# Performance work log

Hardware: AMD Instinct MI355X
Metric: run time of the kernel (lower is better)

The kernel has to match this reference:

```python
import jax, jax.numpy as jnp
import numpy as np


def setup_inputs() -> dict:
    key = jax.random.key(0)
    k1, k2, k3, k4, k5 = jax.random.split(key, 5)
    B, C, G, H, W = 2, 64, 4, 64, 64
    CG = C * G            # 256 complex input channels (flattened)
    DQK = max(C // 8, 1)  # 8  query/key channels after gabor pooling
    scale = 1.0 / np.sqrt(CG)
    x = jax.random.normal(k1, (2, B, C, G, H, W), dtype=jnp.float32)
    wq = jax.random.normal(k2, (2, DQK, CG), dtype=jnp.float32) * scale
    wk = jax.random.normal(k3, (2, DQK, CG), dtype=jnp.float32) * scale
    wv = jax.random.normal(k4, (2, CG, CG), dtype=jnp.float32) * scale
    gamma = jax.random.normal(k5, (1,), dtype=jnp.float32) * 0.1
    return {"x": x, "wq": wq, "wk": wk, "wv": wv, "gamma": gamma}


def _cconv1x1(w, xr, xi):
    """Complex 1x1 conv: (wr+i wi)(xr+i xi). w: (2,O,Cin), x: (B,Cin,L)."""
    wr, wi = w[0], w[1]
    yr = jnp.einsum('oc,bcl->bol', wr, xr) - jnp.einsum('oc,bcl->bol', wi, xi)
    yi = jnp.einsum('oc,bcl->bol', wr, xi) + jnp.einsum('oc,bcl->bol', wi, xr)
    return yr, yi


def reference(x, wq, wk, wv, gamma):
    _, B, C, G, H, W = x.shape
    L = H * W
    xr = x[0].reshape(B, C * G, L)
    xi = x[1].reshape(B, C * G, L)
    # complex Q (B,d,L) / K (B,d,L)
    qr, qi = _cconv1x1(wq, xr, xi)
    kr, ki = _cconv1x1(wk, xr, xi)
    # energy = Q^H-free complex bmm: energy[b,l,m] = sum_d q[b,d,l] * k[b,d,m]
    er = jnp.einsum('bdl,bdm->blm', qr, kr) - jnp.einsum('bdl,bdm->blm', qi, ki)
    ei = jnp.einsum('bdl,bdm->blm', qr, ki) + jnp.einsum('bdl,bdm->blm', qi, kr)
    # magnitude-squared softmax over last axis -> real attention (B,L,L)
    att = jax.nn.softmax(er * er + ei * ei, axis=-1)
    # complex V (B,CG,L); out[b,c,m] = sum_l v[b,c,l] * att[b,m,l]
    vr, vi = _cconv1x1(wv, xr, xi)
    out_r = jnp.einsum('bcl,bml->bcm', vr, att)
    out_i = jnp.einsum('bcl,bml->bcm', vi, att)
    out = jnp.stack([out_r, out_i]).reshape(2, B, C, G, H, W)
    return gamma * out + x
```

## Files before the change

### kernel.cpp

```cpp
#include <hip/hip_runtime.h>
#include <cstdint>

constexpr int Bc  = 2;
constexpr int CGc = 256;
constexpr int Dc  = 8;
constexpr int Lc  = 4096;

typedef __attribute__((ext_vector_type(8))) short short8;
typedef __attribute__((ext_vector_type(4))) float floatx4;

__device__ inline unsigned short f2bf(float f) {
  union { float f; unsigned u; } v; v.f = f;
  unsigned r = v.u + 0x7fffu + ((v.u >> 16) & 1u);
  return (unsigned short)(r >> 16);
}
__device__ inline float bf2f(unsigned short h) {
  return __uint_as_float((unsigned)h << 16);
}

__global__ __launch_bounds__(256) void init_stats(float* __restrict__ p) {
  p[blockIdx.x * 256 + threadIdx.x] = 0.f;
}

__global__ __launch_bounds__(256) void wcat_pack(const float* __restrict__ wv,
                                                 unsigned short* __restrict__ Wcat) {
  const int i  = blockIdx.x * 256 + threadIdx.x;
  const int cc = i >> 9, k = i & 511;
  const int co = cc >> 8, c = cc & 255, ci = k >> 8, cin = k & 255;
  const float wr = wv[(size_t)c * CGc + cin];
  const float wi = wv[(size_t)(CGc + c) * CGc + cin];
  const float val = co == 0 ? (ci == 0 ? wr : -wi) : (ci == 0 ? wi : wr);
  Wcat[i] = f2bf(val);
}

__global__ __launch_bounds__(256) void xT_pack(const float* __restrict__ x,
                                               unsigned short* __restrict__ Xlk) {
  __shared__ float xs[64][65];
  const int tid = threadIdx.x;
  const int b   = blockIdx.z;
  const int l0  = blockIdx.x * 64;
  const int c0  = blockIdx.y * 64;
  const int lt  = tid & 63, r4 = tid >> 6;
#pragma unroll
  for (int p = 0; p < 16; ++p) {
    const int row  = p * 4 + r4;
    const int cin2 = c0 + row;
    const int comp = cin2 >> 8, cin = cin2 & 255;
    xs[row][lt] = x[((size_t)(comp * Bc + b) * CGc + cin) * Lc + l0 + lt];
  }
  __syncthreads();
#pragma unroll
  for (int p = 0; p < 16; ++p) {
    const int lr = p * 4 + r4;
    Xlk[((size_t)b * Lc + l0 + lr) * 512 + c0 + lt] = f2bf(xs[lt][lr]);
  }
}

__global__ __launch_bounds__(256) void qk_proj(const float* __restrict__ x,
                                               const float* __restrict__ wq,
                                               const float* __restrict__ wk,
                                               float* __restrict__ qout,
                                               float* __restrict__ kout) {
  __shared__ float ws[4 * Dc * CGc];
  const int tid = threadIdx.x;
  const int b   = blockIdx.y;
  for (int i = tid; i < 2 * Dc * CGc; i += 256) {
    ws[i]                 = wq[i];
    ws[2 * Dc * CGc + i]  = wk[i];
  }
  __syncthreads();
  const int d  = tid >> 5;
  const int ml = tid & 31;
  const int m  = blockIdx.x * 32 + ml;
  const float* xr = x + ((size_t)(0 * Bc + b) * CGc) * Lc + m;
  const float* xi = x + ((size_t)(1 * Bc + b) * CGc) * Lc + m;
  const float* wqr = ws + d * CGc;
  const float* wqi = ws + (Dc + d) * CGc;
  const float* wkr = ws + 2 * Dc * CGc + d * CGc;
  const float* wki = ws + 2 * Dc * CGc + (Dc + d) * CGc;
  float qer = 0.f, qei = 0.f, ker = 0.f, kei = 0.f;
#pragma unroll 4
  for (int cin = 0; cin < CGc; ++cin) {
    const float vr = xr[(size_t)cin * Lc];
    const float vi = xi[(size_t)cin * Lc];
    const float a1 = wqr[cin], b1 = wqi[cin];
    qer = fmaf(a1, vr, qer); qer = fmaf(-b1, vi, qer);
    qei = fmaf(a1, vi, qei); qei = fmaf(b1, vr, qei);
    const float a2 = wkr[cin], b2 = wki[cin];
    ker = fmaf(a2, vr, ker); ker = fmaf(-b2, vi, ker);
    kei = fmaf(a2, vi, kei); kei = fmaf(b2, vr, kei);
  }
  float* qp = qout + ((size_t)b * Lc + m) * 16;
  qp[d]     = qer;
  qp[8 + d] = qei;
  float* kp = kout + ((size_t)b * Lc + m) * 16;
  kp[d]     = ker;
  kp[8 + d] = kei;
}

__global__ __launch_bounds__(256) void qk_pack(const float* __restrict__ q,
                                               const float* __restrict__ k,
                                               unsigned short* __restrict__ Qcat,
                                               unsigned short* __restrict__ K1hi,
                                               unsigned short* __restrict__ K1lo,
                                               unsigned short* __restrict__ K2hi,
                                               unsigned short* __restrict__ K2lo) {
  const int r = blockIdx.x * 256 + threadIdx.x;
  {
    const float* qp = q + (size_t)r * 16;
    unsigned u[16];
#pragma unroll
    for (int t = 0; t < 8; ++t) {
      const float v0 = qp[2 * t], v1 = qp[2 * t + 1];
      const unsigned short h0 = f2bf(v0), h1 = f2bf(v1);
      u[t] = (unsigned)h0 | ((unsigned)h1 << 16);
      const unsigned short l0 = f2bf(v0 - bf2f(h0));
      const unsigned short l1 = f2bf(v1 - bf2f(h1));
      u[8 + t] = (unsigned)l0 | ((unsigned)l1 << 16);
    }
    uint4* dst = (uint4*)(Qcat + (size_t)r * 32);
    dst[0] = make_uint4(u[0], u[1], u[2], u[3]);
    dst[1] = make_uint4(u[4], u[5], u[6], u[7]);
    dst[2] = make_uint4(u[8], u[9], u[10], u[11]);
    dst[3] = make_uint4(u[12], u[13], u[14], u[15]);
  }
  {
    const float* kp = k + (size_t)r * 16;
    float k1[16], k2[16];
#pragma unroll
    for (int d = 0; d < 8; ++d) {
      const float kr = kp[d], ki = kp[8 + d];
      k1[d] = kr;  k1[8 + d] = -ki;
      k2[d] = ki;  k2[8 + d] = kr;
    }
    unsigned uh[8], ul[8];
#pragma unroll
    for (int t = 0; t < 8; ++t) {
      const unsigned short h0 = f2bf(k1[2 * t]), h1 = f2bf(k1[2 * t + 1]);
      uh[t] = (unsigned)h0 | ((unsigned)h1 << 16);
      const unsigned short l0 = f2bf(k1[2 * t] - bf2f(h0));
      const unsigned short l1 = f2bf(k1[2 * t + 1] - bf2f(h1));
      ul[t] = (unsigned)l0 | ((unsigned)l1 << 16);
    }
    uint4* dh = (uint4*)(K1hi + (size_t)r * 16);
    dh[0] = make_uint4(uh[0], uh[1], uh[2], uh[3]);
    dh[1] = make_uint4(uh[4], uh[5], uh[6], uh[7]);
    uint4* dl = (uint4*)(K1lo + (size_t)r * 16);
    dl[0] = make_uint4(ul[0], ul[1], ul[2], ul[3]);
    dl[1] = make_uint4(ul[4], ul[5], ul[6], ul[7]);
#pragma unroll
    for (int t = 0; t < 8; ++t) {
      const unsigned short h0 = f2bf(k2[2 * t]), h1 = f2bf(k2[2 * t + 1]);
      uh[t] = (unsigned)h0 | ((unsigned)h1 << 16);
      const unsigned short l0 = f2bf(k2[2 * t] - bf2f(h0));
      const unsigned short l1 = f2bf(k2[2 * t + 1] - bf2f(h1));
      ul[t] = (unsigned)l0 | ((unsigned)l1 << 16);
    }
    uint4* dh2 = (uint4*)(K2hi + (size_t)r * 16);
    dh2[0] = make_uint4(uh[0], uh[1], uh[2], uh[3]);
    dh2[1] = make_uint4(uh[4], uh[5], uh[6], uh[7]);
    uint4* dl2 = (uint4*)(K2lo + (size_t)r * 16);
    dl2[0] = make_uint4(ul[0], ul[1], ul[2], ul[3]);
    dl2[1] = make_uint4(ul[4], ul[5], ul[6], ul[7]);
  }
}

__global__ __launch_bounds__(256) void v_gemm(const unsigned short* __restrict__ Wcat,
                                              const unsigned short* __restrict__ Xlk,
                                              unsigned short* __restrict__ vbf) {
  __shared__ short As[128 * 64];
  __shared__ short Bs[64 * 64];
  const int tid  = threadIdx.x;
  const int b    = blockIdx.z;
  const int cc0  = blockIdx.x * 128;
  const int l0   = blockIdx.y * 64;
  const int wid  = tid >> 6, lane = tid & 63;
  const int wcc  = (wid >> 1) * 64;
  const int wl   = (wid & 1) * 32;
  const int lrow = lane & 15, quad = lane >> 4;
  floatx4 acc[4][2] = {};
  const unsigned short* wsrc = Wcat + (size_t)cc0 * 512;
  const unsigned short* xsrc = Xlk + ((size_t)b * Lc + l0) * 512;
  int s_off[4], g_off[4];
#pragma unroll
  for (int r = 0; r < 4; ++r) {
    const int idx = r * 256 + tid;
    const int row = idx >> 3, ch = idx & 7;
    s_off[r] = row * 64 + (ch ^ (row & 7)) * 8;
    g_off[r] = row * 512 + ch * 8;
  }
  short8 ar[4], br[2];
#pragma unroll
  for (int r = 0; r < 4; ++r) ar[r] = *(const short8*)(wsrc + g_off[r]);
#pragma unroll
  for (int r = 0; r < 2; ++r) br[r] = *(const short8*)(xsrc + g_off[r]);
  for (int k0 = 0; k0 < 512; k0 += 64) {
    __syncthreads();
#pragma unroll
    for (int r = 0; r < 4; ++r) *(short8*)&As[s_off[r]] = ar[r];
#pragma unroll
    for (int r = 0; r < 2; ++r) *(short8*)&Bs[s_off[r]] = br[r];
    __syncthreads();
    if (k0 + 64 < 512) {
#pragma unroll
      for (int r = 0; r < 4; ++r) ar[r] = *(const short8*)(wsrc + g_off[r] + k0 + 64);
#pragma unroll
      for (int r = 0; r < 2; ++r) br[r] = *(const short8*)(xsrc + g_off[r] + k0 + 64);
    }
#pragma unroll
    for (int kk = 0; kk < 64; kk += 32) {
      const int cb = kk >> 3;
      short8 af[4], bf[2];
#pragma unroll
      for (int i = 0; i < 4; ++i)
        af[i] = *(const short8*)&As[(wcc + i * 16 + lrow) * 64 +
                                    ((cb + quad) ^ (lrow & 7)) * 8];
#pragma unroll
      for (int j = 0; j < 2; ++j)
        bf[j] = *(const short8*)&Bs[(wl + j * 16 + lrow) * 64 +
                                    ((cb + quad) ^ (lrow & 7)) * 8];
#pragma unroll
      for (int i = 0; i < 4; ++i)
#pragma unroll
        for (int j = 0; j < 2; ++j)
          acc[i][j] = __builtin_amdgcn_mfma_f32_16x16x32_bf16(af[i], bf[j], acc[i][j], 0, 0, 0);
    }
  }
#pragma unroll
  for (int i = 0; i < 4; ++i) {
    const int ccb = cc0 + wcc + i * 16 + quad * 4;
#pragma unroll
    for (int j = 0; j < 2; ++j) {
      const int l = l0 + wl + j * 16 + lrow;
#pragma unroll
      for (int rg = 0; rg < 4; ++rg)
        vbf[((size_t)b * 512 + ccb + rg) * Lc + l] = f2bf(acc[i][j][rg]);
    }
  }
}

__global__ __launch_bounds__(256) void e_max(const unsigned short* __restrict__ Qcat,
                                             const unsigned short* __restrict__ K1hi,
                                             const unsigned short* __restrict__ K2hi,
                                             float* __restrict__ Mrow) {
  const int tid  = threadIdx.x;
  const int w    = tid >> 6, lane = tid & 63;
  const int lrow = lane & 15, quad = lane >> 4, qsel = quad & 1;
  const int b    = blockIdx.z;
  const int m16  = blockIdx.x * 64 + w * 16;
  const int lbeg = blockIdx.y * 512;
  const size_t kb = (size_t)b * Lc;
  const short8 afrag = *(const short8*)(Qcat + (kb + m16 + lrow) * 32 + quad * 8);
  float mx[4] = {0.f, 0.f, 0.f, 0.f};
  for (int l0 = lbeg; l0 < lbeg + 512; l0 += 16) {
    const size_t l = kb + l0 + lrow;
    const short8 b1h = *(const short8*)(K1hi + l * 16 + qsel * 8);
    const short8 b2h = *(const short8*)(K2hi + l * 16 + qsel * 8);
    const floatx4 er = __builtin_amdgcn_mfma_f32_16x16x32_bf16(afrag, b1h, (floatx4){0.f, 0.f, 0.f, 0.f}, 0, 0, 0);
    const floatx4 ei = __builtin_amdgcn_mfma_f32_16x16x32_bf16(afrag, b2h, (floatx4){0.f, 0.f, 0.f, 0.f}, 0, 0, 0);
#pragma unroll
    for (int r = 0; r < 4; ++r) {
      float e = er[r] * er[r];
      e = fmaf(ei[r], ei[r], e);
      mx[r] = fmaxf(mx[r], e);
    }
  }
#pragma unroll
  for (int r = 0; r < 4; ++r) {
    float v = mx[r];
#pragma unroll
    for (int off = 1; off < 16; off <<= 1) v = fmaxf(v, __shfl_xor(v, off));
    if (lrow == 0)
      atomicMax((unsigned*)&Mrow[kb + m16 + quad * 4 + r], __float_as_uint(v));
  }
}

__global__ __launch_bounds__(256) void e_exp(const unsigned short* __restrict__ Qcat,
                                             const unsigned short* __restrict__ K1hi,
                                             const unsigned short* __restrict__ K1lo,
                                             const unsigned short* __restrict__ K2hi,
                                             const unsigned short* __restrict__ K2lo,
                                             const float* __restrict__ Mrow,
                                             unsigned short* __restrict__ att,
                                             float* __restrict__ Ssum) {
  const int tid  = threadIdx.x;
  const int w    = tid >> 6, lane = tid & 63;
  const int lrow = lane & 15, quad = lane >> 4, qsel = quad & 1;
  const int b    = blockIdx.z;
  const int m16  = blockIdx.x * 64 + w * 16;
  const int lbeg = blockIdx.y * 512;
  const size_t kb = (size_t)b * Lc;
  const short8 afrag = *(const short8*)(Qcat + (kb + m16 + lrow) * 32 + quad * 8);
  float Mv[4], sum[4] = {};
#pragma unroll
  for (int r = 0; r < 4; ++r) Mv[r] = Mrow[kb + m16 + quad * 4 + r];
  for (int l0 = lbeg; l0 < lbeg + 512; l0 += 16) {
    const size_t l = kb + l0 + lrow;
    const short8 b1h = *(const short8*)(K1hi + l * 16 + qsel * 8);
    const short8 b1l = *(const short8*)(K1lo + l * 16 + qsel * 8);
    const short8 b2h = *(const short8*)(K2hi + l * 16 + qsel * 8);
    const short8 b2l = *(const short8*)(K2lo + l * 16 + qsel * 8);
    floatx4 er = __builtin_amdgcn_mfma_f32_16x16x32_bf16(afrag, b1l, (floatx4){0.f, 0.f, 0.f, 0.f}, 0, 0, 0);
    er = __builtin_amdgcn_mfma_f32_16x16x32_bf16(afrag, b1h, er, 0, 0, 0);
    floatx4 ei = __builtin_amdgcn_mfma_f32_16x16x32_bf16(afrag, b2l, (floatx4){0.f, 0.f, 0.f, 0.f}, 0, 0, 0);
    ei = __builtin_amdgcn_mfma_f32_16x16x32_bf16(afrag, b2h, ei, 0, 0, 0);
#pragma unroll
    for (int r = 0; r < 4; ++r) {
      float e = er[r] * er[r];
      e = fmaf(ei[r], ei[r], e);
      const float wgt = __expf(e - Mv[r]);
      sum[r] += wgt;
      att[(kb + m16 + quad * 4 + r) * Lc + l0 + lrow] = f2bf(wgt);
    }
  }
#pragma unroll
  for (int r = 0; r < 4; ++r) {
    float v = sum[r];
#pragma unroll
    for (int off = 1; off < 16; off <<= 1) v += __shfl_xor(v, off);
    if (lrow == 0) atomicAdd(&Ssum[kb + m16 + quad * 4 + r], v);
  }
}

__device__ __forceinline__ void pv_compute(const short* __restrict__ As,
                                           const short* __restrict__ Bs,
                                           int wcc, int wm, int lrow, int quad,
                                           floatx4 (&acc)[4][4]) {
#pragma unroll
  for (int kk = 0; kk < 64; kk += 32) {
    const int cb = kk >> 3;
    short8 af[4], bf[4];
#pragma unroll
    for (int i = 0; i < 4; ++i)
      af[i] = *(const short8*)&As[(wcc + i * 16 + lrow) * 64 +
                                  ((cb + quad) ^ (lrow & 7)) * 8];
#pragma unroll
    for (int j = 0; j < 4; ++j)
      bf[j] = *(const short8*)&Bs[(wm + j * 16 + lrow) * 64 +
                                  ((cb + quad) ^ (lrow & 7)) * 8];
#pragma unroll
    for (int i = 0; i < 4; ++i)
#pragma unroll
      for (int j = 0; j < 4; ++j)
        acc[i][j] = __builtin_amdgcn_mfma_f32_16x16x32_bf16(af[i], bf[j], acc[i][j], 0, 0, 0);
  }
}

__global__ __launch_bounds__(512, 2) void pv_gemm(const unsigned short* __restrict__ v,
                                                  const unsigned short* __restrict__ att,
                                                  const float* __restrict__ Ssum,
                                                  const float* __restrict__ x,
                                                  const float* __restrict__ gamma,
                                                  float* __restrict__ out) {
  __shared__ short smem[4 * 128 * 64];
  const int flat = blockIdx.x;
  const int swz  = (flat & 7) * 32 + (flat >> 3);
  const int b    = swz >> 7;
  const int rem  = swz & 127;
  const int m0   = (rem >> 2) * 128;
  const int cc0  = (rem & 3) * 128;
  const int tid  = threadIdx.x;
  const int wid  = tid >> 6, lane = tid & 63;
  const int g    = wid >> 2;
  const int w4   = wid & 3;
  const int wcc  = (w4 >> 1) * 64;
  const int wm   = (w4 & 1) * 64;
  const int lrow = lane & 15, quad = lane >> 4;
  floatx4 acc[4][4] = {};
  const unsigned short* vsrc = v   + ((size_t)b * 512 + cc0) * Lc;
  const unsigned short* asrc = att + ((size_t)b * Lc + m0) * Lc;
  int s_off[2];
  size_t g_off[2];
#pragma unroll
  for (int r = 0; r < 2; ++r) {
    const int c   = r * 512 + tid;
    const int row = c >> 3, ch = c & 7;
    s_off[r] = row * 64 + (ch ^ (row & 7)) * 8;
    g_off[r] = (size_t)row * Lc + ch * 8;
  }
  short8 ar[2][2], br[2][2];
#pragma unroll
  for (int p = 0; p < 2; ++p)
#pragma unroll
    for (int r = 0; r < 2; ++r) {
      ar[p][r] = *(const short8*)(vsrc + g_off[r] + p * 64);
      br[p][r] = *(const short8*)(asrc + g_off[r] + p * 64);
    }
  for (int k0 = 0; k0 < Lc; k0 += 128) {
    __syncthreads();
#pragma unroll
    for (int p = 0; p < 2; ++p)
#pragma unroll
      for (int r = 0; r < 2; ++r) {
        *(short8*)&smem[p * 8192 + s_off[r]]         = ar[p][r];
        *(short8*)&smem[16384 + p * 8192 + s_off[r]] = br[p][r];
      }
    __syncthreads();
    if (k0 + 128 < Lc) {
#pragma unroll
      for (int p = 0; p < 2; ++p)
#pragma unroll
        for (int r = 0; r < 2; ++r) {
          ar[p][r] = *(const short8*)(vsrc + g_off[r] + k0 + 128 + p * 64);
          br[p][r] = *(const short8*)(asrc + g_off[r] + k0 + 128 + p * 64);
        }
    }
    pv_compute(smem + g * 8192, smem + 16384 + g * 8192, wcc, wm, lrow, quad, acc);
  }
  __syncthreads();
  float* red = (float*)smem;
  if (g == 1) {
#pragma unroll
    for (int i = 0; i < 4; ++i)
#pragma unroll
      for (int j = 0; j < 4; ++j) {
        const int tq = i * 4 + j;
        *(floatx4*)&red[((w4 * 64 + lane) * 16 + (tq ^ (lane & 15))) * 4] = acc[i][j];
      }
  }
  __syncthreads();
  if (g == 0) {
#pragma unroll
    for (int i = 0; i < 4; ++i)
#pragma unroll
      for (int j = 0; j < 4; ++j) {
        const int tq = i * 4 + j;
        const floatx4 o = *(const floatx4*)&red[((w4 * 64 + lane) * 16 + (tq ^ (lane & 15))) * 4];
        acc[i][j] += o;
      }
    const float gm = gamma[0];
    float svj[4];
#pragma unroll
    for (int j = 0; j < 4; ++j)
      svj[j] = gm / Ssum[(size_t)b * Lc + m0 + wm + j * 16 + lrow];
#pragma unroll
    for (int i = 0; i < 4; ++i) {
      const int ccb = cc0 + wcc + i * 16 + quad * 4;
#pragma unroll
      for (int j = 0; j < 4; ++j) {
        const int m = m0 + wm + j * 16 + lrow;
#pragma unroll
        for (int rg = 0; rg < 4; ++rg) {
          const int cc   = ccb + rg;
          const int comp = cc >> 8, c = cc & 255;
          const size_t idx = (((size_t)comp * Bc + b) * CGc + c) * Lc + m;
          out[idx] = svj[j] * acc[i][j][rg] + x[idx];
        }
      }
    }
  }
}

extern "C" void kernel_launch(void* const* d_in, const int* in_sizes, int n_in,
                              void* d_out, int out_size, void* d_ws, size_t ws_size,
                              hipStream_t stream) {
  const float* x     = (const float*)d_in[0];
  const float* wq    = (const float*)d_in[1];
  const float* wk    = (const float*)d_in[2];
  const float* wv    = (const float*)d_in[3];
  const float* gamma = (const float*)d_in[4];
  float* out = (float*)d_out;

  float* q    = (float*)d_ws;
  float* kk   = q    + (size_t)Bc * Lc * 16;
  float* Mrow = kk   + (size_t)Bc * Lc * 16;
  float* Ssum = Mrow + (size_t)Bc * Lc;
  unsigned short* vbf  = (unsigned short*)(Ssum + (size_t)Bc * Lc);
  unsigned short* att  = vbf + (size_t)Bc * 512 * Lc;
  unsigned short* Xlk  = att;
  unsigned short* Qcat = att + (size_t)Bc * Lc * Lc;
  unsigned short* K1hi = Qcat + (size_t)Bc * Lc * 32;
  unsigned short* K1lo = K1hi + (size_t)Bc * Lc * 16;
  unsigned short* K2hi = K1lo + (size_t)Bc * Lc * 16;
  unsigned short* K2lo = K2hi + (size_t)Bc * Lc * 16;
  unsigned short* Wcat = K2lo + (size_t)Bc * Lc * 16;

  init_stats<<<dim3((2 * Bc * Lc) / 256), 256, 0, stream>>>(Mrow);
  wcat_pack<<<dim3((512 * 512) / 256), 256, 0, stream>>>(wv, Wcat);
  qk_proj<<<dim3(Lc / 32, Bc), 256, 0, stream>>>(x, wq, wk, q, kk);
  qk_pack<<<dim3((Bc * Lc) / 256), 256, 0, stream>>>(q, kk, Qcat, K1hi, K1lo, K2hi, K2lo);
  xT_pack<<<dim3(Lc / 64, 8, Bc), 256, 0, stream>>>(x, Xlk);
  v_gemm<<<dim3(512 / 128, Lc / 64, Bc), 256, 0, stream>>>(Wcat, Xlk, vbf);
  e_max<<<dim3(Lc / 64, 8, Bc), 256, 0, stream>>>(Qcat, K1hi, K2hi, Mrow);
  e_exp<<<dim3(Lc / 64, 8, Bc), 256, 0, stream>>>(Qcat, K1hi, K1lo, K2hi, K2lo, Mrow, att, Ssum);
  pv_gemm<<<dim3(256), 512, 0, stream>>>(vbf, att, Ssum, x, gamma, out);
}
```

Baseline: 203.5 us.

## Stream PV GEMM tiles directly into LDS with double buffering

The PV GEMM main loop now uses global_load_lds to copy V and attention tiles straight from global memory into a double-buffered LDS region, replacing the register-staged copy. K steps shrink from 128 to 64 per iteration, and the two warp groups split each 64-wide slice by k-halves instead of taking separate 64-wide tiles. This is meant to cut register pressure and VGPR-to-LDS store instructions and to overlap the next tile's load with MFMA work. In exchange it adds twice as many barriers and full vmcnt waits per iteration, which may expose memory latency.

After: 208.8 us. +2.6%, slower.

```diff
diff --git a/kernel.cpp b/kernel.cpp
--- a/kernel.cpp
+++ b/kernel.cpp
@@ -322,28 +322,44 @@
   }
 }
 
-__device__ __forceinline__ void pv_compute(const short* __restrict__ As,
-                                           const short* __restrict__ Bs,
-                                           int wcc, int wm, int lrow, int quad,
-                                           floatx4 (&acc)[4][4]) {
-#pragma unroll
-  for (int kk = 0; kk < 64; kk += 32) {
-    const int cb = kk >> 3;
-    short8 af[4], bf[4];
-#pragma unroll
-    for (int i = 0; i < 4; ++i)
-      af[i] = *(const short8*)&As[(wcc + i * 16 + lrow) * 64 +
-                                  ((cb + quad) ^ (lrow & 7)) * 8];
+__device__ __forceinline__ void pv_stage(const unsigned short* __restrict__ vsrc,
+                                         const unsigned short* __restrict__ asrc,
+                                         short* lds_buf, int k0, int wid, int lane) {
+  const int rsub = lane >> 3;
+  const int ch   = (lane & 7) ^ rsub;
+#pragma unroll
+  for (int t = 0; t < 4; ++t) {
+    const int q    = wid * 4 + t;
+    const int tile = q >> 4;
+    const int j    = q & 15;
+    const int row  = j * 8 + rsub;
+    const unsigned short* g =
+        (tile == 0 ? vsrc : asrc) + (size_t)row * Lc + k0 + ch * 8;
+    short* l = lds_buf + tile * 8192 + j * 512;
+    __builtin_amdgcn_global_load_lds(
+        (const __attribute__((address_space(1))) void*)g,
+        (__attribute__((address_space(3))) void*)l, 16, 0, 0);
+  }
+}
+
+__device__ __forceinline__ void pv_compute32(const short* __restrict__ As,
+                                             const short* __restrict__ Bs,
+                                             int cb, int wcc, int wm, int lrow, int quad,
+                                             floatx4 (&acc)[4][4]) {
+  short8 af[4], bf[4];
+#pragma unroll
+  for (int i = 0; i < 4; ++i)
+    af[i] = *(const short8*)&As[(wcc + i * 16 + lrow) * 64 +
+                                ((cb + quad) ^ (lrow & 7)) * 8];
+#pragma unroll
+  for (int j = 0; j < 4; ++j)
+    bf[j] = *(const short8*)&Bs[(wm + j * 16 + lrow) * 64 +
+                                ((cb + quad) ^ (lrow & 7)) * 8];
+#pragma unroll
+  for (int i = 0; i < 4; ++i)
 #pragma unroll
     for (int j = 0; j < 4; ++j)
-      bf[j] = *(const short8*)&Bs[(wm + j * 16 + lrow) * 64 +
-                                  ((cb + quad) ^ (lrow & 7)) * 8];
-#pragma unroll
-    for (int i = 0; i < 4; ++i)
-#pragma unroll
-      for (int j = 0; j < 4; ++j)
-        acc[i][j] = __builtin_amdgcn_mfma_f32_16x16x32_bf16(af[i], bf[j], acc[i][j], 0, 0, 0);
-  }
+      acc[i][j] = __builtin_amdgcn_mfma_f32_16x16x32_bf16(af[i], bf[j], acc[i][j], 0, 0, 0);
 }
 
 __global__ __launch_bounds__(512, 2) void pv_gemm(const unsigned short* __restrict__ v,
@@ -352,7 +368,7 @@
                                                   const float* __restrict__ x,
                                                   const float* __restrict__ gamma,
                                                   float* __restrict__ out) {
-  __shared__ short smem[4 * 128 * 64];
+  __shared__ short smem[2 * 2 * 128 * 64];
   const int flat = blockIdx.x;
   const int swz  = (flat & 7) * 32 + (flat >> 3);
   const int b    = swz >> 7;
@@ -366,48 +382,22 @@
   const int wcc  = (w4 >> 1) * 64;
   const int wm   = (w4 & 1) * 64;
   const int lrow = lane & 15, quad = lane >> 4;
+  const int cb   = g * 4;
   floatx4 acc[4][4] = {};
   const unsigned short* vsrc = v   + ((size_t)b * 512 + cc0) * Lc;
   const unsigned short* asrc = att + ((size_t)b * Lc + m0) * Lc;
-  int s_off[2];
-  size_t g_off[2];
-#pragma unroll
-  for (int r = 0; r < 2; ++r) {
-    const int c   = r * 512 + tid;
-    const int row = c >> 3, ch = c & 7;
-    s_off[r] = row * 64 + (ch ^ (row & 7)) * 8;
-    g_off[r] = (size_t)row * Lc + ch * 8;
-  }
-  short8 ar[2][2], br[2][2];
-#pragma unroll
-  for (int p = 0; p < 2; ++p)
-#pragma unroll
-    for (int r = 0; r < 2; ++r) {
-      ar[p][r] = *(const short8*)(vsrc + g_off[r] + p * 64);
-      br[p][r] = *(const short8*)(asrc + g_off[r] + p * 64);
-    }
-  for (int k0 = 0; k0 < Lc; k0 += 128) {
+  pv_stage(vsrc, asrc, smem, 0, wid, lane);
+  asm volatile("s_waitcnt vmcnt(0)");
+  __syncthreads();
+  for (int p = 0; p < 64; ++p) {
+    const int cur = p & 1;
+    if (p + 1 < 64)
+      pv_stage(vsrc, asrc, smem + (cur ^ 1) * 16384, (p + 1) * 64, wid, lane);
+    pv_compute32(smem + cur * 16384, smem + cur * 16384 + 8192,
+                 cb, wcc, wm, lrow, quad, acc);
+    asm volatile("s_waitcnt vmcnt(0)");
     __syncthreads();
-#pragma unroll
-    for (int p = 0; p < 2; ++p)
-#pragma unroll
-      for (int r = 0; r < 2; ++r) {
-        *(short8*)&smem[p * 8192 + s_off[r]]         = ar[p][r];
-        *(short8*)&smem[16384 + p * 8192 + s_off[r]] = br[p][r];
-      }
-    __syncthreads();
-    if (k0 + 128 < Lc) {
-#pragma unroll
-      for (int p = 0; p < 2; ++p)
-#pragma unroll
-        for (int r = 0; r < 2; ++r) {
-          ar[p][r] = *(const short8*)(vsrc + g_off[r] + k0 + 128 + p * 64);
-          br[p][r] = *(const short8*)(asrc + g_off[r] + k0 + 128 + p * 64);
-        }
-    }
-    pv_compute(smem + g * 8192, smem + 16384 + g * 8192, wcc, wm, lrow, quad, acc);
-  }
-  __syncthreads();
+  }
   float* red = (float*)smem;
   if (g == 1) {
 #pragma unroll
```
